# Kernel optimization log

Hardware: AMD Instinct MI355X
Metric: run time of the kernel (lower is better)

Reference implementation:

```python
import jax, jax.numpy as jnp
import numpy as np
from jax import lax

ALPHA = 2.0        # elastic_alpha per axis
SMOOTH_NUM = 4
WIN = 5            # box smoothing window
FS = 11            # elastic field size per dim
SIZE_O = (128, 128, 128)


def _rodrigues(rot):
    # rot: (N,3) angle-axis -> (N,3,3) rotation matrix, with Taylor fallback near 0
    eps = 1e-6
    theta2 = jnp.sum(rot * rot, axis=1, keepdims=True)            # (N,1)
    theta = jnp.sqrt(jnp.maximum(theta2, eps))                    # safe sqrt
    w = rot / (theta + eps)
    wx, wy, wz = w[:, 0:1], w[:, 1:2], w[:, 2:3]
    c = jnp.cos(theta)
    s = jnp.sin(theta)
    k = 1.0 - c
    Rn = jnp.concatenate([
        c + wx * wx * k, wx * wy * k - wz * s, wy * s + wx * wz * k,
        wz * s + wx * wy * k, c + wy * wy * k, -wx * s + wy * wz * k,
        -wy * s + wx * wz * k, wx * s + wy * wz * k, c + wz * wz * k,
    ], axis=1).reshape(-1, 3, 3)
    rx, ry, rz = rot[:, 0:1], rot[:, 1:2], rot[:, 2:3]
    one = jnp.ones_like(rx)
    Rt = jnp.concatenate([one, -rz, ry, rz, one, -rx, -ry, rx, one],
                         axis=1).reshape(-1, 3, 3)
    mask = (theta2 > eps)[:, :, None]                             # (N,1,1)
    return jnp.where(mask, Rn, Rt)


def _box_smooth(d):
    # replicate-pad + mean box filter (torch __smooth_3d__)
    p = WIN // 2
    dp = jnp.pad(d, ((0, 0), (0, 0), (p, p), (p, p), (p, p)), mode='edge')
    k = jnp.ones((1, 1, WIN, WIN, WIN), d.dtype) / float(WIN ** 3)
    return lax.conv_general_dilated(dp, k, (1, 1, 1), 'VALID',
                                    dimension_numbers=('NCDHW', 'OIDHW', 'NCDHW'))


def _resize1d(x, axis, out_size):
    # linear interpolation along one axis, align_corners=False (torch interpolate)
    in_size = x.shape[axis]
    src = (jnp.arange(out_size, dtype=x.dtype) + 0.5) * (in_size / out_size) - 0.5
    src = jnp.clip(src, 0.0, in_size - 1.0)
    i0 = jnp.floor(src).astype(jnp.int32)
    i1 = jnp.minimum(i0 + 1, in_size - 1)
    w = (src - i0.astype(x.dtype))
    shape = [1] * x.ndim
    shape[axis] = out_size
    w = w.reshape(shape)
    x0 = jnp.take(x, i0, axis=axis)
    x1 = jnp.take(x, i1, axis=axis)
    return x0 * (1.0 - w) + x1 * w


def _resize3d(d, size):
    d = _resize1d(d, 2, size[0])
    d = _resize1d(d, 3, size[1])
    d = _resize1d(d, 4, size[2])
    return d


def _grid_sample3d(vol, grid):
    # vol: (N,C,D,H,W), grid: (N,D,H,W,3) normalized (x,y,z); trilinear, zeros pad,
    # align_corners=False (torch grid_sample defaults)
    N, C, D, H, W = vol.shape
    x = ((grid[..., 0] + 1.0) * W - 1.0) * 0.5
    y = ((grid[..., 1] + 1.0) * H - 1.0) * 0.5
    z = ((grid[..., 2] + 1.0) * D - 1.0) * 0.5
    x0f, y0f, z0f = jnp.floor(x), jnp.floor(y), jnp.floor(z)
    wx, wy, wz = x - x0f, y - y0f, z - z0f
    x0 = x0f.astype(jnp.int32)
    y0 = y0f.astype(jnp.int32)
    z0 = z0f.astype(jnp.int32)
    b = jnp.arange(N)[:, None, None, None]

    def gather(zi, yi, xi):
        valid = (zi >= 0) & (zi < D) & (yi >= 0) & (yi < H) & (xi >= 0) & (xi < W)
        v = vol[b, :, jnp.clip(zi, 0, D - 1), jnp.clip(yi, 0, H - 1),
                jnp.clip(xi, 0, W - 1)]                           # (N,Do,Ho,Wo,C)
        return v * valid[..., None].astype(vol.dtype)

    out = (gather(z0, y0, x0) * ((1 - wz) * (1 - wy) * (1 - wx))[..., None]
           + gather(z0, y0, x0 + 1) * ((1 - wz) * (1 - wy) * wx)[..., None]
           + gather(z0, y0 + 1, x0) * ((1 - wz) * wy * (1 - wx))[..., None]
           + gather(z0, y0 + 1, x0 + 1) * ((1 - wz) * wy * wx)[..., None]
           + gather(z0 + 1, y0, x0) * (wz * (1 - wy) * (1 - wx))[..., None]
           + gather(z0 + 1, y0, x0 + 1) * (wz * (1 - wy) * wx)[..., None]
           + gather(z0 + 1, y0 + 1, x0) * (wz * wy * (1 - wx))[..., None]
           + gather(z0 + 1, y0 + 1, x0 + 1) * (wz * wy * wx)[..., None])
    return jnp.transpose(out, (0, 4, 1, 2, 3))


def _field(raw, size):
    # raw uniform field -> scaled, smoothed, cropped, resized displacement (D,H,W)
    d = (raw - 0.5) * 2.0 * ALPHA
    for _ in range(SMOOTH_NUM):
        d = _box_smooth(d)
    p = WIN // 2
    d = d[:, :, p:p + FS, p:p + FS, p:p + FS]
    return _resize3d(d, size)[0, 0]


def _forward(vol, rot, scale, shift, dz, dy, dx):
    N, C, D, H, W = vol.shape
    R = _rodrigues(rot)                                  # (N,3,3)
    A = R * scale[:, None, :]                            # scale multiplies columns
    theta = jnp.concatenate([A, shift[:, :, None]], axis=2)  # (N,3,4)
    # base affine grid, align_corners=False: coord_i = (2i+1)/S - 1
    xs = (2.0 * jnp.arange(W, dtype=vol.dtype) + 1.0) / W - 1.0
    ys = (2.0 * jnp.arange(H, dtype=vol.dtype) + 1.0) / H - 1.0
    zs = (2.0 * jnp.arange(D, dtype=vol.dtype) + 1.0) / D - 1.0
    zz, yy, xx = jnp.meshgrid(zs, ys, xs, indexing='ij')
    pts = jnp.stack([xx, yy, zz, jnp.ones_like(xx)], axis=-1)    # (D,H,W,4)
    grid = jnp.einsum('nij,dhwj->ndhwi', theta, pts)             # (N,D,H,W,3)
    disp = jnp.stack([_field(dz, (D, H, W)), _field(dy, (D, H, W)),
                      _field(dx, (D, H, W))], axis=-1)           # (D,H,W,3)
    grid = grid + disp[None]
    out = _grid_sample3d(vol, grid)
    # central crop to SIZE_O
    zs0 = D // 2 - SIZE_O[0] // 2
    ys0 = H // 2 - SIZE_O[1] // 2
    xs0 = W // 2 - SIZE_O[2] // 2
    return out[:, :, zs0:zs0 + SIZE_O[0], ys0:ys0 + SIZE_O[1], xs0:xs0 + SIZE_O[2]]


def setup_inputs() -> dict:
    key = jax.random.key(0)
    k = jax.random.split(key, 7)
    vol = jax.random.normal(k[0], (4, 1, 160, 160, 160), dtype=jnp.float32)
    rot = (jax.random.uniform(k[1], (4, 3), dtype=jnp.float32) - 0.5) * 0.35   # ~±10 deg in rad
    scale = 0.9 + 0.2 * jax.random.uniform(k[2], (4, 3), dtype=jnp.float32)
    shift = (jax.random.uniform(k[3], (4, 3), dtype=jnp.float32) - 0.5) * 0.1
    dz = jax.random.uniform(k[4], (1, 1, 15, 15, 15), dtype=jnp.float32)
    dy = jax.random.uniform(k[5], (1, 1, 15, 15, 15), dtype=jnp.float32)
    dx = jax.random.uniform(k[6], (1, 1, 15, 15, 15), dtype=jnp.float32)
    return {"vol": vol, "rot": rot, "scale": scale, "shift": shift,
            "dz": dz, "dy": dy, "dx": dx}


def reference(vol, rot, scale, shift, dz, dy, dx):
    return _forward(vol, rot, scale, shift, dz, dy, dx)
```

## Files before the change

### kernel.cpp

```cpp
#include <hip/hip_runtime.h>
#include <hip/hip_bf16.h>

#define VD 160
#define OD 128
#define CROP0 16
#define FSZ 11
#define RAWSZ 15
#define NBATCH 4
#define ODQ 4

#define ESTR 17
#define EOH  (8*ESTR)
#define ECH  (8*8*ESTR)

__global__ __launch_bounds__(256) void prep_kernel(
        const float* __restrict__ rot, const float* __restrict__ scale,
        const float* __restrict__ shift,
        const float* __restrict__ dz, const float* __restrict__ dy,
        const float* __restrict__ dx,
        float* __restrict__ theta, float* __restrict__ fields) {
    const int tid = threadIdx.x;
    const int chan = blockIdx.x;

    if (chan == 3) {
        int n = tid;
        if (n >= NBATCH) return;
        float rx = rot[n*3+0], ry = rot[n*3+1], rz = rot[n*3+2];
        float t2 = rx*rx + ry*ry + rz*rz;
        const float eps = 1e-6f;
        float th = sqrtf(fmaxf(t2, eps));
        float inv = 1.0f / (th + eps);
        float wx = rx*inv, wy = ry*inv, wz = rz*inv;
        float c = cosf(th), s = sinf(th), k = 1.0f - c;
        float R[9];
        if (t2 > eps) {
            R[0] = c + wx*wx*k;      R[1] = wx*wy*k - wz*s;  R[2] = wy*s + wx*wz*k;
            R[3] = wz*s + wx*wy*k;   R[4] = c + wy*wy*k;     R[5] = -wx*s + wy*wz*k;
            R[6] = -wy*s + wx*wz*k;  R[7] = wx*s + wy*wz*k;  R[8] = c + wz*wz*k;
        } else {
            R[0] = 1.0f; R[1] = -rz;  R[2] = ry;
            R[3] = rz;   R[4] = 1.0f; R[5] = -rx;
            R[6] = -ry;  R[7] = rx;   R[8] = 1.0f;
        }
        for (int i = 0; i < 3; ++i) {
            for (int j = 0; j < 3; ++j)
                theta[n*12 + i*4 + j] = R[i*3 + j] * scale[n*3 + j];
            theta[n*12 + i*4 + 3] = shift[n*3 + i];
        }
        return;
    }

    __shared__ float bufA[RAWSZ*RAWSZ*RAWSZ];
    __shared__ float bufB[RAWSZ*RAWSZ*RAWSZ];
    const float* raw = (chan == 0) ? dz : (chan == 1) ? dy : dx;
    const int NTOT = RAWSZ*RAWSZ*RAWSZ;

    for (int i = tid; i < NTOT; i += 256)
        bufA[i] = (raw[i] - 0.5f) * 4.0f;
    __syncthreads();

    float* src = bufA;
    float* dst = bufB;
    for (int it = 0; it < 4; ++it) {
        for (int ax = 0; ax < 3; ++ax) {
            const int stride = (ax == 0) ? RAWSZ*RAWSZ : (ax == 1) ? RAWSZ : 1;
            for (int i = tid; i < NTOT; i += 256) {
                int z = i / (RAWSZ*RAWSZ);
                int r = i % (RAWSZ*RAWSZ);
                int y = r / RAWSZ;
                int x = r % RAWSZ;
                int c = (ax == 0) ? z : (ax == 1) ? y : x;
                float s = 0.0f;
                #pragma unroll
                for (int t = -2; t <= 2; ++t) {
                    int cc = min(max(c + t, 0), RAWSZ - 1);
                    s += src[i + (cc - c) * stride];
                }
                dst[i] = s * 0.2f;
            }
            __syncthreads();
            float* tmp = src; src = dst; dst = tmp;
        }
    }
    for (int i = tid; i < FSZ*FSZ*FSZ; i += 256) {
        int z = i / (FSZ*FSZ);
        int r = i % (FSZ*FSZ);
        int y = r / FSZ;
        int x = r % FSZ;
        fields[chan*FSZ*FSZ*FSZ + i] =
            src[(z+2)*RAWSZ*RAWSZ + (y+2)*RAWSZ + (x+2)];
    }
}

__device__ __forceinline__ void resize_coord(int m, int& i0, int& i1, float& w) {
    float s = fmaf((float)m + 0.5f, (float)FSZ / (float)VD, -0.5f);
    s = fminf(fmaxf(s, 0.0f), (float)(FSZ - 1));
    float f = floorf(s);
    i0 = (int)f;
    i1 = min(i0 + 1, FSZ - 1);
    w = s - f;
}

__global__ __launch_bounds__(512) void sample_kernel(
        const float* __restrict__ vol, const float* __restrict__ theta,
        const float* __restrict__ fields, float* __restrict__ out) {
    __shared__ float e[3*ECH];

    const int tid  = threadIdx.x;
    const int lane = tid & 63;
    const int wl   = lane & 15;
    const int hl   = lane >> 4;
    const int wv   = tid >> 6;
    const int wx   = wv & 1;
    const int wh   = (wv >> 1) & 1;
    const int wd   = wv >> 2;

    const int ow_l = (wx << 4) | wl;
    const int oh_l = (wh << 2) | hl;
    const int ow   = (blockIdx.x << 5) | ow_l;
    const int oh   = (blockIdx.y << 3) | oh_l;
    const int odb  = (blockIdx.z & 15) << 3;
    const int n    = blockIdx.z >> 4;

    #pragma unroll
    for (int i = 0; i < 6; ++i) {
        const int t = tid + (i << 9);
        const int xi  = t & 15;
        const int row = t >> 4;
        if (xi < FSZ) {
            const int c   = row >> 6;
            const int r   = row & 63;
            const int eoh = r >> 3;
            const int eod = r & 7;
            int d_ = odb + eod + CROP0;
            int h_ = (blockIdx.y << 3) + eoh + CROP0;
            int zi0, zi1, yi0, yi1;
            float zw, yw;
            resize_coord(d_, zi0, zi1, zw);
            resize_coord(h_, yi0, yi1, yw);
            const float* f = fields + c * (FSZ*FSZ*FSZ);
            float v = f[zi0*121 + yi0*11 + xi] * ((1.0f-zw)*(1.0f-yw))
                    + f[zi0*121 + yi1*11 + xi] * ((1.0f-zw)*yw)
                    + f[zi1*121 + yi0*11 + xi] * (zw*(1.0f-yw))
                    + f[zi1*121 + yi1*11 + xi] * (zw*yw);
            e[row*ESTR + xi] = v * 80.0f;
        }
    }
    __syncthreads();

    const int w_ = ow + CROP0;
    const int h_ = oh + CROP0;

    const float x = fmaf(2.0f * (float)w_ + 1.0f, 1.0f / (float)VD, -1.0f);
    const float y = fmaf(2.0f * (float)h_ + 1.0f, 1.0f / (float)VD, -1.0f);

    float s = fmaf((float)w_ + 0.5f, (float)FSZ / (float)VD, -0.5f);
    s = fminf(fmaxf(s, 0.0f), (float)(FSZ - 1));
    const float sf = floorf(s);
    const int   xi0 = (int)sf;
    const float xw  = s - sf;

    const float* th = theta + n*12;
    const float cx = fmaf(th[0]*x + th[1]*y + th[3], 80.0f, 79.5f);
    const float cy = fmaf(th[4]*x + th[5]*y + th[7], 80.0f, 79.5f);
    const float cz = fmaf(th[8]*x + th[9]*y + th[11], 80.0f, 79.5f);
    const float tz0 = th[2] * 80.0f, tz1 = th[6] * 80.0f, tz2 = th[10] * 80.0f;

    const float* v = vol + (size_t)n * (VD*VD*VD);

    const float* ebase = &e[oh_l*EOH + (wd << 2)*ESTR + xi0];

    #pragma unroll
    for (int k = 0; k < ODQ; ++k) {
        const int od = odb + ((wd << 2) | k);
        const int d_ = od + CROP0;
        const float z = fmaf(2.0f * (float)d_ + 1.0f, 1.0f / (float)VD, -1.0f);

        const float ex0 = ebase[        k*ESTR    ], ex1 = ebase[        k*ESTR + 1];
        const float ey0 = ebase[ECH   + k*ESTR    ], ey1 = ebase[ECH   + k*ESTR + 1];
        const float ez0 = ebase[2*ECH + k*ESTR    ], ez1 = ebase[2*ECH + k*ESTR + 1];
        const float d80x = fmaf(ex1 - ex0, xw, ex0);
        const float d80y = fmaf(ey1 - ey0, xw, ey0);
        const float d80z = fmaf(ez1 - ez0, xw, ez0);

        const float xs = fmaf(tz0, z, cx) + d80x;
        const float ys = fmaf(tz1, z, cy) + d80y;
        const float zs = fmaf(tz2, z, cz) + d80z;

        const float x0f = floorf(xs), y0f = floorf(ys), z0f = floorf(zs);
        const float fx = xs - x0f, fy = ys - y0f, fz = zs - z0f;
        const int ix0 = (int)x0f, iy0 = (int)y0f, iz0 = (int)z0f;
        const int ix1 = ix0 + 1,  iy1 = iy0 + 1,  iz1 = iz0 + 1;

        const float WX0 = ((unsigned)ix0 < (unsigned)VD) ? (1.0f - fx) : 0.0f;
        const float WX1 = ((unsigned)ix1 < (unsigned)VD) ? fx          : 0.0f;
        const float WY0 = ((unsigned)iy0 < (unsigned)VD) ? (1.0f - fy) : 0.0f;
        const float WY1 = ((unsigned)iy1 < (unsigned)VD) ? fy          : 0.0f;
        const float WZ0 = ((unsigned)iz0 < (unsigned)VD) ? (1.0f - fz) : 0.0f;
        const float WZ1 = ((unsigned)iz1 < (unsigned)VD) ? fz          : 0.0f;

        const int xc0 = min(max(ix0, 0), VD-1), xc1 = min(max(ix1, 0), VD-1);
        const int yc0 = min(max(iy0, 0), VD-1), yc1 = min(max(iy1, 0), VD-1);
        const int zc0 = min(max(iz0, 0), VD-1), zc1 = min(max(iz1, 0), VD-1);

        const int base = min(xc0, VD-2);
        const bool hi0 = (xc0 != base);
        const bool hi1 = (xc1 != base);
        const float wA = (hi0 ? 0.0f : WX0) + (hi1 ? 0.0f : WX1);
        const float wB = (hi0 ? WX0 : 0.0f) + (hi1 ? WX1 : 0.0f);

        const int b00 = (zc0*VD + yc0)*VD + base;
        const int b01 = (zc0*VD + yc1)*VD + base;
        const int b10 = (zc1*VD + yc0)*VD + base;
        const int b11 = (zc1*VD + yc1)*VD + base;

        float2 p00, p01, p10, p11;
        __builtin_memcpy(&p00, v + b00, sizeof(float2));
        __builtin_memcpy(&p01, v + b01, sizeof(float2));
        __builtin_memcpy(&p10, v + b10, sizeof(float2));
        __builtin_memcpy(&p11, v + b11, sizeof(float2));

        const float r00 = p00.x*wA + p00.y*wB;
        const float r01 = p01.x*wA + p01.y*wB;
        const float r10 = p10.x*wA + p10.y*wB;
        const float r11 = p11.x*wA + p11.y*wB;
        const float r = (r00*WY0 + r01*WY1)*WZ0 + (r10*WY0 + r11*WY1)*WZ1;

        out[(((size_t)n*OD + od)*OD + oh)*OD + ow] = r;
    }
}

extern "C" void kernel_launch(void* const* d_in, const int* in_sizes, int n_in,
                              void* d_out, int out_size, void* d_ws, size_t ws_size,
                              hipStream_t stream) {
    const float* vol   = (const float*)d_in[0];
    const float* rot   = (const float*)d_in[1];
    const float* scale = (const float*)d_in[2];
    const float* shift = (const float*)d_in[3];
    const float* dz    = (const float*)d_in[4];
    const float* dy    = (const float*)d_in[5];
    const float* dx    = (const float*)d_in[6];
    float* out = (float*)d_out;

    float* ws     = (float*)d_ws;
    float* theta  = ws;
    float* fields = ws + 48;

    prep_kernel<<<4, 256, 0, stream>>>(rot, scale, shift, dz, dy, dx,
                                       theta, fields);
    dim3 grid(OD/32, OD/8, (OD/8)*NBATCH);
    sample_kernel<<<grid, 512, 0, stream>>>(vol, theta, fields, out);
}
```

Measured before the change: 160.5 us.

## Precompute z/y-resized elastic field in prep kernel, load it with float4

The prep kernel now runs 96 blocks. Each block redoes the small box smoothing and then writes a precomputed (od,oh) grid of z/y-interpolated, pre-scaled displacement rows for all three channels into global workspace. The sample kernel copies these rows into shared memory with coalesced float4 loads, replacing per-block bilinear gathers and index math. The cost is 96 blocks each repeating the smoothing, about 2.4 MB of extra workspace traffic, and a larger prep launch on the critical path.

```diff
diff --git a/kernel.cpp b/kernel.cpp
--- a/kernel.cpp
+++ b/kernel.cpp
@@ -9,20 +9,20 @@
 #define NBATCH 4
 #define ODQ 4
 
-#define ESTR 17
-#define EOH  (8*ESTR)
-#define ECH  (8*8*ESTR)
+#define EGC 12
+#define EGP 36
+#define NSLICE 32
 
 __global__ __launch_bounds__(256) void prep_kernel(
         const float* __restrict__ rot, const float* __restrict__ scale,
         const float* __restrict__ shift,
         const float* __restrict__ dz, const float* __restrict__ dy,
         const float* __restrict__ dx,
-        float* __restrict__ theta, float* __restrict__ fields) {
+        float* __restrict__ theta, float* __restrict__ Eg) {
     const int tid = threadIdx.x;
-    const int chan = blockIdx.x;
-
-    if (chan == 3) {
+    const int bx  = blockIdx.x;
+
+    if (bx == 96) {
         int n = tid;
         if (n >= NBATCH) return;
         float rx = rot[n*3+0], ry = rot[n*3+1], rz = rot[n*3+2];
@@ -49,6 +49,9 @@
         }
         return;
     }
+
+    const int chan  = bx >> 5;
+    const int slice = bx & 31;
 
     __shared__ float bufA[RAWSZ*RAWSZ*RAWSZ];
     __shared__ float bufB[RAWSZ*RAWSZ*RAWSZ];
@@ -82,29 +85,56 @@
             float* tmp = src; src = dst; dst = tmp;
         }
     }
-    for (int i = tid; i < FSZ*FSZ*FSZ; i += 256) {
-        int z = i / (FSZ*FSZ);
-        int r = i % (FSZ*FSZ);
-        int y = r / FSZ;
-        int x = r % FSZ;
-        fields[chan*FSZ*FSZ*FSZ + i] =
-            src[(z+2)*RAWSZ*RAWSZ + (y+2)*RAWSZ + (x+2)];
-    }
-}
-
-__device__ __forceinline__ void resize_coord(int m, int& i0, int& i1, float& w) {
-    float s = fmaf((float)m + 0.5f, (float)FSZ / (float)VD, -0.5f);
-    s = fminf(fmaxf(s, 0.0f), (float)(FSZ - 1));
-    float f = floorf(s);
-    i0 = (int)f;
-    i1 = min(i0 + 1, FSZ - 1);
-    w = s - f;
+
+    for (int p = slice*512 + tid; p < slice*512 + 512; p += 256) {
+        const int od = p >> 7;
+        const int oh = p & 127;
+        const int d_ = od + CROP0;
+        const int h_ = oh + CROP0;
+
+        float sz = fmaf((float)d_ + 0.5f, (float)FSZ / (float)VD, -0.5f);
+        sz = fminf(fmaxf(sz, 0.0f), (float)(FSZ - 1));
+        float szf = floorf(sz);
+        int   zi0 = (int)szf;
+        int   zi1 = min(zi0 + 1, FSZ - 1);
+        float zw  = sz - szf;
+
+        float sy = fmaf((float)h_ + 0.5f, (float)FSZ / (float)VD, -0.5f);
+        sy = fminf(fmaxf(sy, 0.0f), (float)(FSZ - 1));
+        float syf = floorf(sy);
+        int   yi0 = (int)syf;
+        int   yi1 = min(yi0 + 1, FSZ - 1);
+        float yw  = sy - syf;
+
+        const float w00 = (1.0f-zw)*(1.0f-yw) * 80.0f;
+        const float w01 = (1.0f-zw)*yw * 80.0f;
+        const float w10 = zw*(1.0f-yw) * 80.0f;
+        const float w11 = zw*yw * 80.0f;
+
+        const float* r00 = src + (zi0+2)*(RAWSZ*RAWSZ) + (yi0+2)*RAWSZ + 2;
+        const float* r01 = src + (zi0+2)*(RAWSZ*RAWSZ) + (yi1+2)*RAWSZ + 2;
+        const float* r10 = src + (zi1+2)*(RAWSZ*RAWSZ) + (yi0+2)*RAWSZ + 2;
+        const float* r11 = src + (zi1+2)*(RAWSZ*RAWSZ) + (yi1+2)*RAWSZ + 2;
+
+        float vbuf[EGC];
+        #pragma unroll
+        for (int xi = 0; xi < FSZ; ++xi)
+            vbuf[xi] = r00[xi]*w00 + r01[xi]*w01 + r10[xi]*w10 + r11[xi]*w11;
+        vbuf[11] = vbuf[10];
+
+        float* dstp = Eg + (size_t)p*EGP + chan*EGC;
+        #pragma unroll
+        for (int q = 0; q < 3; ++q) {
+            float4 f4 = make_float4(vbuf[4*q], vbuf[4*q+1], vbuf[4*q+2], vbuf[4*q+3]);
+            __builtin_memcpy(dstp + 4*q, &f4, sizeof(float4));
+        }
+    }
 }
 
 __global__ __launch_bounds__(512) void sample_kernel(
         const float* __restrict__ vol, const float* __restrict__ theta,
-        const float* __restrict__ fields, float* __restrict__ out) {
-    __shared__ float e[3*ECH];
+        const float* __restrict__ Eg, float* __restrict__ out) {
+    __shared__ float e[8*8*EGP];
 
     const int tid  = threadIdx.x;
     const int lane = tid & 63;
@@ -119,32 +149,17 @@
     const int oh_l = (wh << 2) | hl;
     const int ow   = (blockIdx.x << 5) | ow_l;
     const int oh   = (blockIdx.y << 3) | oh_l;
+    const int ohb  = blockIdx.y << 3;
     const int odb  = (blockIdx.z & 15) << 3;
     const int n    = blockIdx.z >> 4;
 
-    #pragma unroll
-    for (int i = 0; i < 6; ++i) {
-        const int t = tid + (i << 9);
-        const int xi  = t & 15;
-        const int row = t >> 4;
-        if (xi < FSZ) {
-            const int c   = row >> 6;
-            const int r   = row & 63;
-            const int eoh = r >> 3;
-            const int eod = r & 7;
-            int d_ = odb + eod + CROP0;
-            int h_ = (blockIdx.y << 3) + eoh + CROP0;
-            int zi0, zi1, yi0, yi1;
-            float zw, yw;
-            resize_coord(d_, zi0, zi1, zw);
-            resize_coord(h_, yi0, yi1, yw);
-            const float* f = fields + c * (FSZ*FSZ*FSZ);
-            float v = f[zi0*121 + yi0*11 + xi] * ((1.0f-zw)*(1.0f-yw))
-                    + f[zi0*121 + yi1*11 + xi] * ((1.0f-zw)*yw)
-                    + f[zi1*121 + yi0*11 + xi] * (zw*(1.0f-yw))
-                    + f[zi1*121 + yi1*11 + xi] * (zw*yw);
-            e[row*ESTR + xi] = v * 80.0f;
-        }
+    for (int t = tid; t < 8*72; t += 512) {
+        const int od_l = t / 72;
+        const int r    = t - od_l*72;
+        const float* g = Eg + ((size_t)(odb + od_l)*128 + ohb)*EGP + 4*r;
+        float4 f4;
+        __builtin_memcpy(&f4, g, sizeof(float4));
+        __builtin_memcpy(&e[od_l*288 + 4*r], &f4, sizeof(float4));
     }
     __syncthreads();
 
@@ -168,7 +183,7 @@
 
     const float* v = vol + (size_t)n * (VD*VD*VD);
 
-    const float* ebase = &e[oh_l*EOH + (wd << 2)*ESTR + xi0];
+    const float* ebase = &e[((wd << 2)*8 + oh_l)*EGP + xi0];
 
     #pragma unroll
     for (int k = 0; k < ODQ; ++k) {
@@ -176,9 +191,9 @@
         const int d_ = od + CROP0;
         const float z = fmaf(2.0f * (float)d_ + 1.0f, 1.0f / (float)VD, -1.0f);
 
-        const float ex0 = ebase[        k*ESTR    ], ex1 = ebase[        k*ESTR + 1];
-        const float ey0 = ebase[ECH   + k*ESTR    ], ey1 = ebase[ECH   + k*ESTR + 1];
-        const float ez0 = ebase[2*ECH + k*ESTR    ], ez1 = ebase[2*ECH + k*ESTR + 1];
+        const float ex0 = ebase[k*288          ], ex1 = ebase[k*288           + 1];
+        const float ey0 = ebase[k*288 + EGC    ], ey1 = ebase[k*288 + EGC     + 1];
+        const float ez0 = ebase[k*288 + 2*EGC  ], ez1 = ebase[k*288 + 2*EGC   + 1];
         const float d80x = fmaf(ex1 - ex0, xw, ex0);
         const float d80y = fmaf(ey1 - ey0, xw, ey0);
         const float d80z = fmaf(ez1 - ez0, xw, ez0);
@@ -244,10 +259,10 @@
 
     float* ws     = (float*)d_ws;
     float* theta  = ws;
-    float* fields = ws + 48;
-
-    prep_kernel<<<4, 256, 0, stream>>>(rot, scale, shift, dz, dy, dx,
-                                       theta, fields);
+    float* Eg     = ws + 64;
+
+    prep_kernel<<<97, 256, 0, stream>>>(rot, scale, shift, dz, dy, dx,
+                                        theta, Eg);
     dim3 grid(OD/32, OD/8, (OD/8)*NBATCH);
-    sample_kernel<<<grid, 512, 0, stream>>>(vol, theta, fields, out);
+    sample_kernel<<<grid, 512, 0, stream>>>(vol, theta, Eg, out);
 }
```

After: 162.7 us. About the same (+1.4%).
